# Performance work log

Hardware: AMD Instinct MI355X
Metric: run time of the kernel (lower is better)

## Reference

```python
import jax, jax.numpy as jnp
import numpy as np


def a_powers(A, t):
    # A: [K, n, n]; returns [t, K, n, n] = stack(I, A, A^2, ..., A^(t-1))
    K, n, _ = A.shape
    result = jnp.broadcast_to(jnp.eye(n, dtype=A.dtype), (1, K, n, n))
    lift = A
    while result.shape[0] < t:
        result = jnp.concatenate([result, result @ lift], axis=0)
        lift = lift @ lift
    return result[:t]


def fast_conv_real(a, b):
    # a: [len1, K, n, n], b: [batch, len2, K, n] -> conv(b, a): [batch, len1+len2-1, K, n]
    len1 = a.shape[0]
    len2 = b.shape[1]
    T = 2 ** int(np.ceil(np.log2(len1 + len2 - 1)))
    Af = jnp.fft.rfft(a, n=T, axis=0)
    Bf = jnp.fft.rfft(b, n=T, axis=1)
    Cf = jnp.einsum('blki,lkij->blkj', Bf, Af)
    c = jnp.fft.irfft(Cf, n=T, axis=1)
    return c[:, :len1 + len2 - 1]


def setup_inputs() -> dict:
    key = jax.random.key(0)
    k_u, k_x0, k_theta, k_B, k_C = jax.random.split(key, 5)
    batch, length = 8, 4096
    input_size, state_size, output_size = 256, 256, 256
    blk = 2
    K = state_size // blk  # 128
    u = jax.random.normal(k_u, (batch, length, input_size), dtype=jnp.float32)
    x0 = jax.random.normal(k_x0, (batch, K, blk), dtype=jnp.float32)
    # A initialized as K random 2x2 rotation blocks (as in __init__)
    theta = 2 * jnp.pi * jax.random.uniform(k_theta, (K,), dtype=jnp.float32)
    c, s = jnp.cos(theta), jnp.sin(theta)
    A = jnp.stack([jnp.stack([c, s], -1), jnp.stack([-s, c], -1)], -2)  # [K, 2, 2]
    B = jax.random.normal(k_B, (input_size, state_size), dtype=jnp.float32) / (state_size + input_size) ** 0.5
    C = jax.random.normal(k_C, (state_size, output_size), dtype=jnp.float32) / (state_size + output_size) ** 0.5
    return {"u": u, "x0": x0, "A": A, "B": B, "C": C}


def reference(u, x0, A, B, C):
    batch, length, _ = u.shape
    K, blk, _ = A.shape
    Aps = a_powers(A, length + 1)          # [length+1, K, blk, blk]
    uB = (u @ B).reshape(batch, length, K, blk)
    x = fast_conv_real(Aps[:-1], uB)[:, :length]  # [batch, length, K, blk]
    x = x + jnp.einsum('bki,lkij->blkj', x0, Aps[1:])
    new_state = x[:, -1]                    # [batch, K, blk]
    y = x.reshape(batch, length, K * blk) @ C
    return (y, new_state)
```

## Files before the change

kernel.cpp:

```cpp
#include <hip/hip_runtime.h>
#include <hip/hip_bf16.h>

typedef __bf16 bf16x2_t __attribute__((ext_vector_type(2)));
typedef __bf16 bf16x8_t __attribute__((ext_vector_type(8)));
typedef float f32x4 __attribute__((ext_vector_type(4)));

#define BATCH   8
#define LENGTH  4096
#define KHALF   128
#define MTOT    (BATCH*LENGTH)
#define NCHUNK  128
#define LC      32

#define SWZ(ch, row) ((ch) ^ ((row) & 7))

__global__ __launch_bounds__(256) void transpose_bc(
    const float* __restrict__ Bsrc, const float* __restrict__ Csrc,
    __bf16* __restrict__ BT, __bf16* __restrict__ CT) {
  const float* src = blockIdx.y ? Csrc : Bsrc;
  __bf16* dst      = blockIdx.y ? CT   : BT;
  int n  = blockIdx.x;
  int kk = threadIdx.x;
  dst[n * 256 + kk] = (__bf16)src[kk * 256 + n];
}

__global__ __launch_bounds__(256) void gemm1_fused(
    const float* __restrict__ u, const __bf16* __restrict__ BT,
    const float* __restrict__ Aarr,
    __bf16* __restrict__ uB, float2* __restrict__ P) {
  __shared__ __align__(16) __bf16 sA[128 * 256];

  const int tid  = threadIdx.x;
  const int lane = tid & 63;
  const int wave = tid >> 6;
  const int wr   = wave >> 1, wc = wave & 1;
  const int m_l  = lane & 15, quad = lane >> 4;
  const int m0   = blockIdx.x * 128;
  const int n0   = blockIdx.y * 128;
  const int b    = m0 >> 12;
  const int t0   = m0 & 4095;

#pragma unroll
  for (int i = 0; i < 16; ++i) {
    int s   = tid + i * 256;
    int row = s >> 5, ch = s & 31;
    const float4* g = (const float4*)(u + (size_t)(m0 + row) * 256 + ch * 8);
    float4 a = g[0], c = g[1];
    bf16x8_t v;
    v[0]=(__bf16)a.x; v[1]=(__bf16)a.y; v[2]=(__bf16)a.z; v[3]=(__bf16)a.w;
    v[4]=(__bf16)c.x; v[5]=(__bf16)c.y; v[6]=(__bf16)c.z; v[7]=(__bf16)c.w;
    *(bf16x8_t*)&sA[row * 256 + SWZ(ch, row) * 8] = v;
  }
  __syncthreads();

  f32x4 acc[4][4];
#pragma unroll
  for (int mi = 0; mi < 4; ++mi)
#pragma unroll
    for (int ni = 0; ni < 4; ++ni)
#pragma unroll
      for (int r = 0; r < 4; ++r) acc[mi][ni][r] = 0.f;

#pragma unroll
  for (int kc8 = 0; kc8 < 8; ++kc8) {
    bf16x8_t af[4], bfr[4];
#pragma unroll
    for (int mi = 0; mi < 4; ++mi) {
      int row = wr * 64 + mi * 16 + m_l;
      int c   = kc8 * 4 + quad;
      af[mi] = *(const bf16x8_t*)&sA[row * 256 + SWZ(c, row) * 8];
    }
#pragma unroll
    for (int ni = 0; ni < 4; ++ni) {
      int n = n0 + wc * 64 + ni * 16 + m_l;
      bfr[ni] = *(const bf16x8_t*)(BT + (size_t)n * 256 + kc8 * 32 + quad * 8);
    }
#pragma unroll
    for (int mi = 0; mi < 4; ++mi)
#pragma unroll
      for (int ni = 0; ni < 4; ++ni)
        acc[mi][ni] = __builtin_amdgcn_mfma_f32_16x16x32_bf16(af[mi], bfr[ni], acc[mi][ni], 0, 0, 0);
  }
  __syncthreads();

  __bf16* sT = sA;
#pragma unroll
  for (int mi = 0; mi < 4; ++mi)
#pragma unroll
    for (int ni = 0; ni < 4; ++ni)
#pragma unroll
      for (int r = 0; r < 4; ++r) {
        int row = wr * 64 + mi * 16 + quad * 4 + r;
        int col = wc * 64 + ni * 16 + m_l;
        __bf16 val = (__bf16)acc[mi][ni][r];
        uB[(size_t)(m0 + row) * 256 + n0 + col] = val;
        sT[row * 128 + SWZ(col >> 3, row) * 8 + (col & 7)] = val;
      }
  __syncthreads();

  {
    int kl  = tid & 63;
    int chl = tid >> 6;
    int kg  = (n0 >> 1) + kl;
    float cc = Aarr[4 * kg], sv = Aarr[4 * kg + 1];
    float hr = 0.f, hi = 0.f;
#pragma unroll 8
    for (int j = 0; j < LC; ++j) {
      int row = chl * 32 + j;
      int col = 2 * kl;
      bf16x2_t v2 = *(const bf16x2_t*)&sT[row * 128 + SWZ(col >> 3, row) * 8 + (col & 7)];
      float t = fmaf(hr, cc, fmaf(-hi, sv, (float)v2[0]));
      hi      = fmaf(hr, sv, fmaf( hi, cc, (float)v2[1]));
      hr = t;
    }
    int chg = (t0 >> 5) + chl;
    P[((size_t)b * NCHUNK + chg) * KHALF + kg] = make_float2(hr, hi);
  }
}

__global__ __launch_bounds__(256) void scan_carry2(
    const float* __restrict__ Aarr, const float* __restrict__ x0,
    const float2* __restrict__ P, float2* __restrict__ H,
    float* __restrict__ state_out) {
  const int lane = threadIdx.x & 63;
  const int wv   = threadIdx.x >> 6;
  const int p    = blockIdx.x * 4 + wv;
  const int b    = p >> 7, k = p & 127;
  const float cc = Aarr[4 * k], sv = Aarr[4 * k + 1];

  float wr = cc, wi = sv;
#pragma unroll
  for (int i = 0; i < 5; ++i) { float nr = wr*wr - wi*wi; wi = 2.f*wr*wi; wr = nr; }
  float Wr[6], Wi[6];
  Wr[0] = wr*wr - wi*wi; Wi[0] = 2.f*wr*wi;
#pragma unroll
  for (int s = 1; s < 6; ++s) { Wr[s] = Wr[s-1]*Wr[s-1] - Wi[s-1]*Wi[s-1]; Wi[s] = 2.f*Wr[s-1]*Wi[s-1]; }

  float2 P0 = P[((size_t)b * NCHUNK + 2 * lane)     * KHALF + k];
  float2 P1 = P[((size_t)b * NCHUNK + 2 * lane + 1) * KHALF + k];
  float qr = fmaf(wr, P0.x, fmaf(-wi, P0.y, P1.x));
  float qi = fmaf(wr, P0.y, fmaf( wi, P0.x, P1.y));
  float Sr = qr, Si = qi;
#pragma unroll
  for (int s = 0; s < 6; ++s) {
    float tr = __shfl_up(Sr, 1 << s, 64);
    float ti = __shfl_up(Si, 1 << s, 64);
    if (lane >= (1 << s)) {
      float nSr = fmaf(Wr[s], tr, fmaf(-Wi[s], ti, Sr));
      float nSi = fmaf(Wr[s], ti, fmaf( Wi[s], tr, Si));
      Sr = nSr; Si = nSi;
    }
  }
  float Ar = __shfl_up(Sr, 1, 64), Ai = __shfl_up(Si, 1, 64);
  if (lane == 0) { Ar = 0.f; Ai = 0.f; }
  float pr = 1.f, pi = 0.f;
#pragma unroll
  for (int s = 0; s < 6; ++s)
    if ((lane >> s) & 1) { float nr = pr*Wr[s] - pi*Wi[s]; pi = pr*Wi[s] + pi*Wr[s]; pr = nr; }

  float x0r = x0[b * 256 + 2 * k], x0i = x0[b * 256 + 2 * k + 1];
  float H0r = fmaf(pr, x0r, fmaf(-pi, x0i, Ar));
  float H0i = fmaf(pr, x0i, fmaf( pi, x0r, Ai));
  H[((size_t)b * NCHUNK + 2 * lane) * KHALF + k] = make_float2(H0r, H0i);
  float H1r = fmaf(wr, H0r, fmaf(-wi, H0i, P0.x));
  float H1i = fmaf(wr, H0i, fmaf( wi, H0r, P0.y));
  H[((size_t)b * NCHUNK + 2 * lane + 1) * KHALF + k] = make_float2(H1r, H1i);
  if (lane == 63) {
    state_out[b * 256 + 2 * k]     = fmaf(wr, H1r, fmaf(-wi, H1i, P1.x));
    state_out[b * 256 + 2 * k + 1] = fmaf(wr, H1i, fmaf( wi, H1r, P1.y));
  }
}

__global__ __launch_bounds__(256) void gemm2_fused(
    const __bf16* __restrict__ uB, const float* __restrict__ Aarr,
    const float2* __restrict__ H, const __bf16* __restrict__ CT,
    float* __restrict__ Y) {
  __shared__ __align__(16) __bf16 sX[128 * 256];

  const int tid  = threadIdx.x;
  const int lane = tid & 63;
  const int wave = tid >> 6;
  const int wr   = wave >> 1, wc = wave & 1;
  const int m_l  = lane & 15, quad = lane >> 4;
  const int m0   = blockIdx.x * 128;
  const int n0   = blockIdx.y * 128;
  const int b    = m0 >> 12;
  const int t0   = m0 & 4095;

#pragma unroll
  for (int i = 0; i < 16; ++i) {
    int s   = tid + i * 256;
    int row = s >> 5, ch = s & 31;
    *(bf16x8_t*)&sX[row * 256 + SWZ(ch, row) * 8] =
        *(const bf16x8_t*)(uB + (size_t)(m0 + row) * 256 + ch * 8);
  }
  __syncthreads();

  {
    int k   = tid & 127;
    int ch0 = tid >> 7;
    float cc = Aarr[4 * k], sv = Aarr[4 * k + 1];
#pragma unroll
    for (int pass = 0; pass < 2; ++pass) {
      int chl = ch0 + 2 * pass;
      float2 h = H[((size_t)b * NCHUNK + (t0 >> 5) + chl) * KHALF + k];
      float hr = h.x, hi = h.y;
#pragma unroll 8
      for (int j = 0; j < LC; ++j) {
        int row = chl * 32 + j;
        int idx = row * 256 + SWZ(k >> 2, row) * 8 + ((2 * k) & 7);
        bf16x2_t v2 = *(const bf16x2_t*)&sX[idx];
        float t = fmaf(hr, cc, fmaf(-hi, sv, (float)v2[0]));
        hi      = fmaf(hr, sv, fmaf( hi, cc, (float)v2[1]));
        hr = t;
        bf16x2_t o; o[0] = (__bf16)hr; o[1] = (__bf16)hi;
        *(bf16x2_t*)&sX[idx] = o;
      }
    }
  }
  __syncthreads();

  f32x4 acc[4][4];
#pragma unroll
  for (int mi = 0; mi < 4; ++mi)
#pragma unroll
    for (int ni = 0; ni < 4; ++ni)
#pragma unroll
      for (int r = 0; r < 4; ++r) acc[mi][ni][r] = 0.f;

#pragma unroll
  for (int kc8 = 0; kc8 < 8; ++kc8) {
    bf16x8_t af[4], bfr[4];
#pragma unroll
    for (int mi = 0; mi < 4; ++mi) {
      int row = wr * 64 + mi * 16 + m_l;
      int c   = kc8 * 4 + quad;
      af[mi] = *(const bf16x8_t*)&sX[row * 256 + SWZ(c, row) * 8];
    }
#pragma unroll
    for (int ni = 0; ni < 4; ++ni) {
      int n = n0 + wc * 64 + ni * 16 + m_l;
      bfr[ni] = *(const bf16x8_t*)(CT + (size_t)n * 256 + kc8 * 32 + quad * 8);
    }
#pragma unroll
    for (int mi = 0; mi < 4; ++mi)
#pragma unroll
      for (int ni = 0; ni < 4; ++ni)
        acc[mi][ni] = __builtin_amdgcn_mfma_f32_16x16x32_bf16(af[mi], bfr[ni], acc[mi][ni], 0, 0, 0);
  }

#pragma unroll
  for (int mi = 0; mi < 4; ++mi)
#pragma unroll
    for (int ni = 0; ni < 4; ++ni)
#pragma unroll
      for (int r = 0; r < 4; ++r) {
        int row = m0 + wr * 64 + mi * 16 + quad * 4 + r;
        int col = n0 + wc * 64 + ni * 16 + m_l;
        Y[(size_t)row * 256 + col] = acc[mi][ni][r];
      }
}

extern "C" void kernel_launch(void* const* d_in, const int* in_sizes, int n_in,
                              void* d_out, int out_size, void* d_ws, size_t ws_size,
                              hipStream_t stream) {
  const float* u  = (const float*)d_in[0];
  const float* x0 = (const float*)d_in[1];
  const float* A  = (const float*)d_in[2];
  const float* B  = (const float*)d_in[3];
  const float* C  = (const float*)d_in[4];

  float* y         = (float*)d_out;
  float* state_out = y + (size_t)MTOT * 256;

  char* ws = (char*)d_ws;
  __bf16* BT = (__bf16*)ws;  ws += 256 * 256 * 2;
  __bf16* CT = (__bf16*)ws;  ws += 256 * 256 * 2;
  __bf16* uB = (__bf16*)ws;  ws += (size_t)MTOT * 256 * 2;
  float2* P  = (float2*)ws;  ws += (size_t)BATCH * NCHUNK * KHALF * sizeof(float2);
  float2* H  = (float2*)ws;  ws += (size_t)BATCH * NCHUNK * KHALF * sizeof(float2);

  transpose_bc<<<dim3(256, 2), 256, 0, stream>>>(B, C, BT, CT);
  gemm1_fused<<<dim3(MTOT / 128, 2), 256, 0, stream>>>(u, BT, A, uB, P);
  scan_carry2<<<dim3(256), 256, 0, stream>>>(A, x0, P, H, state_out);
  gemm2_fused<<<dim3(MTOT / 128, 2), 256, 0, stream>>>(uB, A, H, CT, y);
}
```

Baseline: 121.8 us.

## Retile GEMMs to 64 rows by full 256 columns, avoiding duplicated input work

Both fused GEMM kernels change from 128x128 tiles over a 2-wide N grid to 64-row tiles that span all 256 output columns, with each wave owning 64 columns. Previously every row tile of u (and of uB in gemm2) was loaded, converted and, in gemm2, scanned twice, once per N half. Now each row tile is handled by a single block. In gemm1 the uB write-back goes through shared memory as coalesced 16-byte stores instead of scattered bf16 scalar stores, and gemm2's intra-chunk scan becomes one pass per thread. LDS per block halves, which may raise occupancy, while each block reads the full B/C weight matrix.

After: 119.4 us. 2.0% less time.

```diff
diff --git a/kernel.cpp b/kernel.cpp
--- a/kernel.cpp
+++ b/kernel.cpp
@@ -28,20 +28,18 @@
     const float* __restrict__ u, const __bf16* __restrict__ BT,
     const float* __restrict__ Aarr,
     __bf16* __restrict__ uB, float2* __restrict__ P) {
-  __shared__ __align__(16) __bf16 sA[128 * 256];
+  __shared__ __align__(16) __bf16 sA[64 * 256];
 
   const int tid  = threadIdx.x;
   const int lane = tid & 63;
   const int wave = tid >> 6;
-  const int wr   = wave >> 1, wc = wave & 1;
   const int m_l  = lane & 15, quad = lane >> 4;
-  const int m0   = blockIdx.x * 128;
-  const int n0   = blockIdx.y * 128;
+  const int m0   = blockIdx.x * 64;
   const int b    = m0 >> 12;
   const int t0   = m0 & 4095;
 
 #pragma unroll
-  for (int i = 0; i < 16; ++i) {
+  for (int i = 0; i < 8; ++i) {
     int s   = tid + i * 256;
     int row = s >> 5, ch = s & 31;
     const float4* g = (const float4*)(u + (size_t)(m0 + row) * 256 + ch * 8);
@@ -66,13 +64,13 @@
     bf16x8_t af[4], bfr[4];
 #pragma unroll
     for (int mi = 0; mi < 4; ++mi) {
-      int row = wr * 64 + mi * 16 + m_l;
+      int row = mi * 16 + m_l;
       int c   = kc8 * 4 + quad;
       af[mi] = *(const bf16x8_t*)&sA[row * 256 + SWZ(c, row) * 8];
     }
 #pragma unroll
     for (int ni = 0; ni < 4; ++ni) {
-      int n = n0 + wc * 64 + ni * 16 + m_l;
+      int n = wave * 64 + ni * 16 + m_l;
       bfr[ni] = *(const bf16x8_t*)(BT + (size_t)n * 256 + kc8 * 32 + quad * 8);
     }
 #pragma unroll
@@ -90,31 +88,35 @@
     for (int ni = 0; ni < 4; ++ni)
 #pragma unroll
       for (int r = 0; r < 4; ++r) {
-        int row = wr * 64 + mi * 16 + quad * 4 + r;
-        int col = wc * 64 + ni * 16 + m_l;
-        __bf16 val = (__bf16)acc[mi][ni][r];
-        uB[(size_t)(m0 + row) * 256 + n0 + col] = val;
-        sT[row * 128 + SWZ(col >> 3, row) * 8 + (col & 7)] = val;
+        int row = mi * 16 + quad * 4 + r;
+        int col = wave * 64 + ni * 16 + m_l;
+        sT[row * 256 + SWZ(col >> 3, row) * 8 + (col & 7)] = (__bf16)acc[mi][ni][r];
       }
   __syncthreads();
 
+#pragma unroll
+  for (int i = 0; i < 8; ++i) {
+    int s   = tid + i * 256;
+    int row = s >> 5, ch = s & 31;
+    *(bf16x8_t*)(uB + (size_t)(m0 + row) * 256 + ch * 8) =
+        *(const bf16x8_t*)&sT[row * 256 + SWZ(ch, row) * 8];
+  }
+
   {
-    int kl  = tid & 63;
-    int chl = tid >> 6;
-    int kg  = (n0 >> 1) + kl;
-    float cc = Aarr[4 * kg], sv = Aarr[4 * kg + 1];
+    int k   = tid & 127;
+    int chl = tid >> 7;
+    float cc = Aarr[4 * k], sv = Aarr[4 * k + 1];
     float hr = 0.f, hi = 0.f;
 #pragma unroll 8
     for (int j = 0; j < LC; ++j) {
       int row = chl * 32 + j;
-      int col = 2 * kl;
-      bf16x2_t v2 = *(const bf16x2_t*)&sT[row * 128 + SWZ(col >> 3, row) * 8 + (col & 7)];
+      bf16x2_t v2 = *(const bf16x2_t*)&sT[row * 256 + SWZ(k >> 2, row) * 8 + ((2 * k) & 7)];
       float t = fmaf(hr, cc, fmaf(-hi, sv, (float)v2[0]));
       hi      = fmaf(hr, sv, fmaf( hi, cc, (float)v2[1]));
       hr = t;
     }
     int chg = (t0 >> 5) + chl;
-    P[((size_t)b * NCHUNK + chg) * KHALF + kg] = make_float2(hr, hi);
+    P[((size_t)b * NCHUNK + chg) * KHALF + k] = make_float2(hr, hi);
   }
 }
 
@@ -175,20 +177,18 @@
     const __bf16* __restrict__ uB, const float* __restrict__ Aarr,
     const float2* __restrict__ H, const __bf16* __restrict__ CT,
     float* __restrict__ Y) {
-  __shared__ __align__(16) __bf16 sX[128 * 256];
+  __shared__ __align__(16) __bf16 sX[64 * 256];
 
   const int tid  = threadIdx.x;
   const int lane = tid & 63;
   const int wave = tid >> 6;
-  const int wr   = wave >> 1, wc = wave & 1;
   const int m_l  = lane & 15, quad = lane >> 4;
-  const int m0   = blockIdx.x * 128;
-  const int n0   = blockIdx.y * 128;
+  const int m0   = blockIdx.x * 64;
   const int b    = m0 >> 12;
   const int t0   = m0 & 4095;
 
 #pragma unroll
-  for (int i = 0; i < 16; ++i) {
+  for (int i = 0; i < 8; ++i) {
     int s   = tid + i * 256;
     int row = s >> 5, ch = s & 31;
     *(bf16x8_t*)&sX[row * 256 + SWZ(ch, row) * 8] =
@@ -198,24 +198,20 @@
 
   {
     int k   = tid & 127;
-    int ch0 = tid >> 7;
+    int chl = tid >> 7;
     float cc = Aarr[4 * k], sv = Aarr[4 * k + 1];
-#pragma unroll
-    for (int pass = 0; pass < 2; ++pass) {
-      int chl = ch0 + 2 * pass;
-      float2 h = H[((size_t)b * NCHUNK + (t0 >> 5) + chl) * KHALF + k];
-      float hr = h.x, hi = h.y;
+    float2 h = H[((size_t)b * NCHUNK + (t0 >> 5) + chl) * KHALF + k];
+    float hr = h.x, hi = h.y;
 #pragma unroll 8
-      for (int j = 0; j < LC; ++j) {
-        int row = chl * 32 + j;
-        int idx = row * 256 + SWZ(k >> 2, row) * 8 + ((2 * k) & 7);
-        bf16x2_t v2 = *(const bf16x2_t*)&sX[idx];
-        float t = fmaf(hr, cc, fmaf(-hi, sv, (float)v2[0]));
-        hi      = fmaf(hr, sv, fmaf( hi, cc, (float)v2[1]));
-        hr = t;
-        bf16x2_t o; o[0] = (__bf16)hr; o[1] = (__bf16)hi;
-        *(bf16x2_t*)&sX[idx] = o;
-      }
+    for (int j = 0; j < LC; ++j) {
+      int row = chl * 32 + j;
+      int idx = row * 256 + SWZ(k >> 2, row) * 8 + ((2 * k) & 7);
+      bf16x2_t v2 = *(const bf16x2_t*)&sX[idx];
+      float t = fmaf(hr, cc, fmaf(-hi, sv, (float)v2[0]));
+      hi      = fmaf(hr, sv, fmaf( hi, cc, (float)v2[1]));
+      hr = t;
+      bf16x2_t o; o[0] = (__bf16)hr; o[1] = (__bf16)hi;
+      *(bf16x2_t*)&sX[idx] = o;
     }
   }
   __syncthreads();
@@ -233,13 +229,13 @@
     bf16x8_t af[4], bfr[4];
 #pragma unroll
     for (int mi = 0; mi < 4; ++mi) {
-      int row = wr * 64 + mi * 16 + m_l;
+      int row = mi * 16 + m_l;
       int c   = kc8 * 4 + quad;
       af[mi] = *(const bf16x8_t*)&sX[row * 256 + SWZ(c, row) * 8];
     }
 #pragma unroll
     for (int ni = 0; ni < 4; ++ni) {
-      int n = n0 + wc * 64 + ni * 16 + m_l;
+      int n = wave * 64 + ni * 16 + m_l;
       bfr[ni] = *(const bf16x8_t*)(CT + (size_t)n * 256 + kc8 * 32 + quad * 8);
     }
 #pragma unroll
@@ -255,8 +251,8 @@
     for (int ni = 0; ni < 4; ++ni)
 #pragma unroll
       for (int r = 0; r < 4; ++r) {
-        int row = m0 + wr * 64 + mi * 16 + quad * 4 + r;
-        int col = n0 + wc * 64 + ni * 16 + m_l;
+        int row = m0 + mi * 16 + quad * 4 + r;
+        int col = wave * 64 + ni * 16 + m_l;
         Y[(size_t)row * 256 + col] = acc[mi][ni][r];
       }
 }
@@ -281,7 +277,7 @@
   float2* H  = (float2*)ws;  ws += (size_t)BATCH * NCHUNK * KHALF * sizeof(float2);
 
   transpose_bc<<<dim3(256, 2), 256, 0, stream>>>(B, C, BT, CT);
-  gemm1_fused<<<dim3(MTOT / 128, 2), 256, 0, stream>>>(u, BT, A, uB, P);
+  gemm1_fused<<<dim3(MTOT / 64), 256, 0, stream>>>(u, BT, A, uB, P);
   scan_carry2<<<dim3(256), 256, 0, stream>>>(A, x0, P, H, state_out);
-  gemm2_fused<<<dim3(MTOT / 128, 2), 256, 0, stream>>>(uB, A, H, CT, y);
-}
+  gemm2_fused<<<dim3(MTOT / 64), 256, 0, stream>>>(uB, A, H, CT, y);
+}
```
